# Optimization experiments

Measured on AMD Instinct MI355X. Metric: run time of the kernel, lower is better.

## Reference

```python
import jax, jax.numpy as jnp
import numpy as np

EPS = 1e-4          # scn.BatchNormLeakyReLU default eps
LEAKINESS = 0.333   # scn.BatchNormLeakyReLU default leakiness
Z, Y, X = 3, 1280, 2048
N_ACTIVE = 1_500_000
CIN, COUT = 32, 64
KVOL = 4  # filter [1,2,2]


def setup_inputs() -> dict:
    key = jax.random.key(0)
    k1, k2, k3 = jax.random.split(key, 3)
    rng = np.random.default_rng(0)
    flat = rng.choice(Z * Y * X, size=N_ACTIVE, replace=False)
    z = flat // (Y * X)
    rem = flat % (Y * X)
    y = rem // X
    x = rem % X
    # stride==filter_size [1,2,2]: each input hits exactly one output site / offset
    out_flat = z * ((Y // 2) * (X // 2)) + (y // 2) * (X // 2) + (x // 2)
    uniq, inv = np.unique(out_flat, return_inverse=True)
    out_idx = jnp.asarray(inv.astype(np.int32))
    kern_idx = jnp.asarray(((y % 2) * 2 + (x % 2)).astype(np.int32))
    n_out = int(uniq.shape[0])
    features = jax.random.normal(k1, (N_ACTIVE, CIN), dtype=jnp.float32)
    weight = jax.random.normal(k2, (KVOL, CIN, COUT), dtype=jnp.float32) * np.float32(
        np.sqrt(2.0 / (KVOL * CIN)))
    bias = jax.random.normal(k3, (COUT,), dtype=jnp.float32) * 0.01
    gamma = jnp.ones((COUT,), dtype=jnp.float32)
    beta = jnp.zeros((COUT,), dtype=jnp.float32)
    return {"features": features, "weight": weight, "bias": bias,
            "gamma": gamma, "beta": beta, "out_idx": out_idx,
            "kern_idx": kern_idx, "n_out": n_out}


def reference(features, weight, bias, gamma, beta, out_idx, kern_idx, n_out):
    # --- sparse conv: rulebook gather-GEMM-scatter -----------------------
    out = jnp.zeros((n_out, weight.shape[-1]), dtype=features.dtype)
    for k in range(weight.shape[0]):  # fixed kernel volume = 4
        masked = jnp.where((kern_idx == k)[:, None], features, 0.0)
        out = out + jax.ops.segment_sum(masked @ weight[k], out_idx,
                                        num_segments=n_out)
    out = out + bias
    # --- fused BatchNorm (training stats over active sites) + LeakyReLU --
    mean = jnp.mean(out, axis=0)
    var = jnp.mean(jnp.square(out - mean), axis=0)  # biased, as BN
    y = gamma * (out - mean) * jax.lax.rsqrt(var + EPS) + beta
    return jnp.where(y > 0, y, LEAKINESS * y)
```

## Files before the change

kernel.cpp:

```cpp
#include <hip/hip_runtime.h>

#define LEAK 0.333f
#define BN_EPS 1e-4f

typedef __fp16 h2 __attribute__((ext_vector_type(2)));
typedef __fp16 h8 __attribute__((ext_vector_type(8)));
typedef float  f4 __attribute__((ext_vector_type(4)));

union H8 { h2 p[4]; h8 v; };

__global__ __launch_bounds__(256) void fill_table_kernel(
    const int* __restrict__ out_idx, const int* __restrict__ kern_idx,
    int* __restrict__ table, int n_in)
{
    const int i = blockIdx.x * 256 + threadIdx.x;
    if (i < n_in) {
        table[out_idx[i] * 4 + kern_idx[i]] = i;
    }
}

template <bool APPLY>
__global__ __launch_bounds__(256, 2) void conv_pass_kernel(
    const float* __restrict__ feat, const float* __restrict__ weight,
    const int4* __restrict__ table, float* __restrict__ out,
    float* __restrict__ stats, int n_out)
{
    const int lane = threadIdx.x & 63;
    const int wv   = threadIdx.x >> 6;
    const int c    = lane & 15;
    const int g    = lane >> 4;
    const int g8   = g * 8;

    H8 bw[4][4];
#pragma unroll
    for (int s = 0; s < 4; ++s)
#pragma unroll
        for (int n = 0; n < 4; ++n)
#pragma unroll
            for (int e = 0; e < 4; ++e) {
                const int k0 = g8 + 2 * e;
                bw[s][n].p[e] = __builtin_amdgcn_cvt_pkrtz(
                    weight[(s * 32 + k0    ) * 64 + n * 16 + c],
                    weight[(s * 32 + k0 + 1) * 64 + n * 16 + c]);
            }

    float scl[4], sft[4];
    if (APPLY) {
#pragma unroll
        for (int n = 0; n < 4; ++n) {
            scl[n] = stats[128 + n * 16 + c];
            sft[n] = stats[192 + n * 16 + c];
        }
    }

    float sv[4] = {0.f, 0.f, 0.f, 0.f};
    float qv[4] = {0.f, 0.f, 0.f, 0.f};

    const int ntiles  = (n_out + 15) >> 4;
    const int tstride = gridDim.x * 4;
    int t = blockIdx.x * 4 + wv;

    int4 sl  = make_int4(-1, -1, -1, -1);
    int4 sl1 = make_int4(-1, -1, -1, -1);
    f4 va[4][2];
#pragma unroll
    for (int s = 0; s < 4; ++s) { va[s][0] = 0.f; va[s][1] = 0.f; }

    if (t < ntiles) {
        const int row = t * 16 + c;
        if (row < n_out) sl = table[row];
        const int si0[4] = {sl.x, sl.y, sl.z, sl.w};
#pragma unroll
        for (int s = 0; s < 4; ++s) {
            if (si0[s] >= 0) {
                const float* p = feat + (size_t)si0[s] * 32 + g8;
                va[s][0] = *(const f4*)p;
                va[s][1] = *(const f4*)(p + 4);
            }
        }
        const int tn = t + tstride;
        if (tn < ntiles) {
            const int rn = tn * 16 + c;
            if (rn < n_out) sl1 = table[rn];
        }
    }

    for (; t < ntiles; t += tstride) {
        const int tn = t + tstride;

        int4 sl2 = make_int4(-1, -1, -1, -1);
        const int tn2 = tn + tstride;
        if (tn2 < ntiles) {
            const int rn2 = tn2 * 16 + c;
            if (rn2 < n_out) sl2 = table[rn2];
        }

        f4 vb[4][2];
#pragma unroll
        for (int s = 0; s < 4; ++s) { vb[s][0] = 0.f; vb[s][1] = 0.f; }
        if (tn < ntiles) {
            const int si1[4] = {sl1.x, sl1.y, sl1.z, sl1.w};
#pragma unroll
            for (int s = 0; s < 4; ++s) {
                if (si1[s] >= 0) {
                    const float* p = feat + (size_t)si1[s] * 32 + g8;
                    vb[s][0] = *(const f4*)p;
                    vb[s][1] = *(const f4*)(p + 4);
                }
            }
        }

        H8 af[4];
#pragma unroll
        for (int s = 0; s < 4; ++s) {
            af[s].p[0] = __builtin_amdgcn_cvt_pkrtz(va[s][0].x, va[s][0].y);
            af[s].p[1] = __builtin_amdgcn_cvt_pkrtz(va[s][0].z, va[s][0].w);
            af[s].p[2] = __builtin_amdgcn_cvt_pkrtz(va[s][1].x, va[s][1].y);
            af[s].p[3] = __builtin_amdgcn_cvt_pkrtz(va[s][1].z, va[s][1].w);
        }

        f4 acc[4];
#pragma unroll
        for (int n = 0; n < 4; ++n) acc[n] = 0.f;
#pragma unroll
        for (int s = 0; s < 4; ++s)
#pragma unroll
            for (int n = 0; n < 4; ++n)
                acc[n] = __builtin_amdgcn_mfma_f32_16x16x32_f16(
                    af[s].v, bw[s][n].v, acc[n], 0, 0, 0);

        const int rbase = t * 16 + g * 4;
#pragma unroll
        for (int r = 0; r < 4; ++r) {
            const int ro = rbase + r;
            if (APPLY) {
                if (ro < n_out) {
                    float* po = out + (size_t)ro * 64 + c;
#pragma unroll
                    for (int n = 0; n < 4; ++n) {
                        float y = fmaf(acc[n][r], scl[n], sft[n]);
                        po[n * 16] = y > 0.f ? y : LEAK * y;
                    }
                }
            } else {
#pragma unroll
                for (int n = 0; n < 4; ++n) {
                    sv[n] += acc[n][r];
                    qv[n] = fmaf(acc[n][r], acc[n][r], qv[n]);
                }
            }
        }

#pragma unroll
        for (int s = 0; s < 4; ++s) { va[s][0] = vb[s][0]; va[s][1] = vb[s][1]; }
        sl1 = sl2;
    }

    if constexpr (!APPLY) {
#pragma unroll
        for (int n = 0; n < 4; ++n) {
            sv[n] += __shfl_xor(sv[n], 16);
            sv[n] += __shfl_xor(sv[n], 32);
            qv[n] += __shfl_xor(qv[n], 16);
            qv[n] += __shfl_xor(qv[n], 32);
        }

        __shared__ float ls[4][64];
        __shared__ float lq[4][64];
        if (lane < 16) {
#pragma unroll
            for (int n = 0; n < 4; ++n) {
                ls[wv][n * 16 + lane] = sv[n];
                lq[wv][n * 16 + lane] = qv[n];
            }
        }
        __syncthreads();
        if (wv == 0) {
            float ts = ls[0][lane] + ls[1][lane] + ls[2][lane] + ls[3][lane];
            float tq = lq[0][lane] + lq[1][lane] + lq[2][lane] + lq[3][lane];
            atomicAdd(&stats[lane], ts);
            atomicAdd(&stats[64 + lane], tq);
        }
    }
}

__global__ void finalize_kernel(float* __restrict__ stats,
                                const float* __restrict__ gamma,
                                const float* __restrict__ beta, float inv_n)
{
    const int j = threadIdx.x;
    float mean = stats[j] * inv_n;
    float var  = fmaf(-mean, mean, stats[64 + j] * inv_n);
    var = fmaxf(var, 0.f);
    float scale = gamma[j] * rsqrtf(var + BN_EPS);
    stats[128 + j] = scale;
    stats[192 + j] = beta[j] - mean * scale;
}

extern "C" void kernel_launch(void* const* d_in, const int* in_sizes, int n_in,
                              void* d_out, int out_size, void* d_ws, size_t ws_size,
                              hipStream_t stream)
{
    const float* feat     = (const float*)d_in[0];
    const float* weight   = (const float*)d_in[1];
    const float* gamma    = (const float*)d_in[3];
    const float* beta     = (const float*)d_in[4];
    const int*   out_idx  = (const int*)d_in[5];
    const int*   kern_idx = (const int*)d_in[6];
    const int n_active = in_sizes[5];
    const int n_out    = out_size / 64;
    float* out   = (float*)d_out;
    float* stats = (float*)d_ws;
    int*   table = (int*)((char*)d_ws + 1024);

    (void)hipMemsetAsync(stats, 0, 512, stream);
    (void)hipMemsetAsync(table, 0xFF, (size_t)n_out * 4 * sizeof(int), stream);

    fill_table_kernel<<<(n_active + 255) / 256, 256, 0, stream>>>(
        out_idx, kern_idx, table, n_active);
    conv_pass_kernel<false><<<2048, 256, 0, stream>>>(
        feat, weight, (const int4*)table, nullptr, stats, n_out);
    finalize_kernel<<<1, 64, 0, stream>>>(stats, gamma, beta, 1.0f / (float)n_out);
    conv_pass_kernel<true><<<2048, 256, 0, stream>>>(
        feat, weight, (const int4*)table, out, stats, n_out);
}
```

Baseline: 549.4 us.

## Pre-convert features to fp16 once and deepen gather prefetch to two tiles

Adds a conversion kernel that writes the fp32 features to an fp16 copy in workspace once, so both conv passes gather half the bytes per row and skip the per-pass conversion. Missing table entries now read a zeroed row instead of taking a branch, and the software pipeline prefetches two tiles ahead rather than one. The cost is an extra full read of the fp32 features plus a write of the fp16 copy, more workspace, and more registers held for the deeper prefetch.

```diff
diff --git a/kernel.cpp b/kernel.cpp
--- a/kernel.cpp
+++ b/kernel.cpp
@@ -19,11 +19,28 @@
     }
 }
 
+__global__ __launch_bounds__(256) void convert_kernel(
+    const f4* __restrict__ in, H8* __restrict__ out16, int n8)
+{
+    int i = blockIdx.x * 256 + threadIdx.x;
+    const int stride = gridDim.x * 256;
+    for (; i < n8; i += stride) {
+        f4 a = in[2 * i];
+        f4 b = in[2 * i + 1];
+        H8 o;
+        o.p[0] = __builtin_amdgcn_cvt_pkrtz(a.x, a.y);
+        o.p[1] = __builtin_amdgcn_cvt_pkrtz(a.z, a.w);
+        o.p[2] = __builtin_amdgcn_cvt_pkrtz(b.x, b.y);
+        o.p[3] = __builtin_amdgcn_cvt_pkrtz(b.z, b.w);
+        out16[i] = o;
+    }
+}
+
 template <bool APPLY>
 __global__ __launch_bounds__(256, 2) void conv_pass_kernel(
-    const float* __restrict__ feat, const float* __restrict__ weight,
-    const int4* __restrict__ table, float* __restrict__ out,
-    float* __restrict__ stats, int n_out)
+    const __fp16* __restrict__ f16, const float* __restrict__ weight,
+    const int4* __restrict__ table, const __fp16* __restrict__ zrow,
+    float* __restrict__ out, float* __restrict__ stats, int n_out)
 {
     const int lane = threadIdx.x & 63;
     const int wv   = threadIdx.x >> 6;
@@ -57,67 +74,35 @@
     float qv[4] = {0.f, 0.f, 0.f, 0.f};
 
     const int ntiles  = (n_out + 15) >> 4;
-    const int tstride = gridDim.x * 4;
-    int t = blockIdx.x * 4 + wv;
-
-    int4 sl  = make_int4(-1, -1, -1, -1);
-    int4 sl1 = make_int4(-1, -1, -1, -1);
-    f4 va[4][2];
-#pragma unroll
-    for (int s = 0; s < 4; ++s) { va[s][0] = 0.f; va[s][1] = 0.f; }
-
-    if (t < ntiles) {
-        const int row = t * 16 + c;
-        if (row < n_out) sl = table[row];
-        const int si0[4] = {sl.x, sl.y, sl.z, sl.w};
-#pragma unroll
-        for (int s = 0; s < 4; ++s) {
-            if (si0[s] >= 0) {
-                const float* p = feat + (size_t)si0[s] * 32 + g8;
-                va[s][0] = *(const f4*)p;
-                va[s][1] = *(const f4*)(p + 4);
-            }
-        }
-        const int tn = t + tstride;
-        if (tn < ntiles) {
-            const int rn = tn * 16 + c;
-            if (rn < n_out) sl1 = table[rn];
-        }
-    }
-
-    for (; t < ntiles; t += tstride) {
-        const int tn = t + tstride;
-
-        int4 sl2 = make_int4(-1, -1, -1, -1);
-        const int tn2 = tn + tstride;
-        if (tn2 < ntiles) {
-            const int rn2 = tn2 * 16 + c;
-            if (rn2 < n_out) sl2 = table[rn2];
-        }
-
-        f4 vb[4][2];
-#pragma unroll
-        for (int s = 0; s < 4; ++s) { vb[s][0] = 0.f; vb[s][1] = 0.f; }
-        if (tn < ntiles) {
-            const int si1[4] = {sl1.x, sl1.y, sl1.z, sl1.w};
-#pragma unroll
-            for (int s = 0; s < 4; ++s) {
-                if (si1[s] >= 0) {
-                    const float* p = feat + (size_t)si1[s] * 32 + g8;
-                    vb[s][0] = *(const f4*)p;
-                    vb[s][1] = *(const f4*)(p + 4);
-                }
-            }
-        }
-
-        H8 af[4];
-#pragma unroll
-        for (int s = 0; s < 4; ++s) {
-            af[s].p[0] = __builtin_amdgcn_cvt_pkrtz(va[s][0].x, va[s][0].y);
-            af[s].p[1] = __builtin_amdgcn_cvt_pkrtz(va[s][0].z, va[s][0].w);
-            af[s].p[2] = __builtin_amdgcn_cvt_pkrtz(va[s][1].x, va[s][1].y);
-            af[s].p[3] = __builtin_amdgcn_cvt_pkrtz(va[s][1].z, va[s][1].w);
-        }
+    const int ts      = gridDim.x * 4;
+    const int t0      = blockIdx.x * 4 + wv;
+
+    auto loadtab = [&](int x) -> int4 {
+        int4 r = make_int4(-1, -1, -1, -1);
+        if (x < ntiles) {
+            const int row = x * 16 + c;
+            if (row < n_out) r = table[row];
+        }
+        return r;
+    };
+    auto ld = [&](int si) -> h8 {
+        const __fp16* p = (si >= 0) ? (f16 + ((size_t)si * 32 + g8))
+                                    : (zrow + g8);
+        return *(const h8*)p;
+    };
+
+    int4 tb2 = loadtab(t0 + 2 * ts);
+    int4 tbA = loadtab(t0);
+    int4 tbB = loadtab(t0 + ts);
+
+    h8 fA[4], fB[4];
+    fA[0] = ld(tbA.x); fA[1] = ld(tbA.y); fA[2] = ld(tbA.z); fA[3] = ld(tbA.w);
+    fB[0] = ld(tbB.x); fB[1] = ld(tbB.y); fB[2] = ld(tbB.z); fB[3] = ld(tbB.w);
+
+    for (int t = t0; t < ntiles; t += ts) {
+        int4 tb3 = loadtab(t + 3 * ts);
+        h8 fC[4];
+        fC[0] = ld(tb2.x); fC[1] = ld(tb2.y); fC[2] = ld(tb2.z); fC[3] = ld(tb2.w);
 
         f4 acc[4];
 #pragma unroll
@@ -127,7 +112,7 @@
 #pragma unroll
             for (int n = 0; n < 4; ++n)
                 acc[n] = __builtin_amdgcn_mfma_f32_16x16x32_f16(
-                    af[s].v, bw[s][n].v, acc[n], 0, 0, 0);
+                    fA[s], bw[s][n].v, acc[n], 0, 0, 0);
 
         const int rbase = t * 16 + g * 4;
 #pragma unroll
@@ -152,8 +137,8 @@
         }
 
 #pragma unroll
-        for (int s = 0; s < 4; ++s) { va[s][0] = vb[s][0]; va[s][1] = vb[s][1]; }
-        sl1 = sl2;
+        for (int s = 0; s < 4; ++s) { fA[s] = fB[s]; fB[s] = fC[s]; }
+        tb2 = tb3;
     }
 
     if constexpr (!APPLY) {
@@ -176,10 +161,10 @@
         }
         __syncthreads();
         if (wv == 0) {
-            float ts = ls[0][lane] + ls[1][lane] + ls[2][lane] + ls[3][lane];
-            float tq = lq[0][lane] + lq[1][lane] + lq[2][lane] + lq[3][lane];
-            atomicAdd(&stats[lane], ts);
-            atomicAdd(&stats[64 + lane], tq);
+            float ts2 = ls[0][lane] + ls[1][lane] + ls[2][lane] + ls[3][lane];
+            float tq2 = lq[0][lane] + lq[1][lane] + lq[2][lane] + lq[3][lane];
+            atomicAdd(&stats[lane], ts2);
+            atomicAdd(&stats[64 + lane], tq2);
         }
     }
 }
@@ -210,17 +195,23 @@
     const int n_active = in_sizes[5];
     const int n_out    = out_size / 64;
     float* out   = (float*)d_out;
-    float* stats = (float*)d_ws;
-    int*   table = (int*)((char*)d_ws + 1024);
-
-    (void)hipMemsetAsync(stats, 0, 512, stream);
+
+    float*  stats = (float*)d_ws;
+    __fp16* zrow  = (__fp16*)((char*)d_ws + 1024);
+    int*    table = (int*)((char*)d_ws + 2048);
+    size_t  f16_off = 2048 + (((size_t)n_out * 16 + 255) & ~(size_t)255);
+    __fp16* f16   = (__fp16*)((char*)d_ws + f16_off);
+
+    (void)hipMemsetAsync(d_ws, 0, 1088, stream);
     (void)hipMemsetAsync(table, 0xFF, (size_t)n_out * 4 * sizeof(int), stream);
 
     fill_table_kernel<<<(n_active + 255) / 256, 256, 0, stream>>>(
         out_idx, kern_idx, table, n_active);
+    convert_kernel<<<2048, 256, 0, stream>>>(
+        (const f4*)feat, (H8*)f16, n_active * 4);
     conv_pass_kernel<false><<<2048, 256, 0, stream>>>(
-        feat, weight, (const int4*)table, nullptr, stats, n_out);
+        f16, weight, (const int4*)table, zrow, nullptr, stats, n_out);
     finalize_kernel<<<1, 64, 0, stream>>>(stats, gamma, beta, 1.0f / (float)n_out);
     conv_pass_kernel<true><<<2048, 256, 0, stream>>>(
-        feat, weight, (const int4*)table, out, stats, n_out);
-}
+        f16, weight, (const int4*)table, zrow, out, stats, n_out);
+}
```

After: 589.7 us. 1.07x slower.
